# Kernel optimization log

Hardware: AMD Instinct MI355X
Metric: run time of the kernel (lower is better)

## Reference

```python
import jax, jax.numpy as jnp
import numpy as np
from jax import lax

MAX_DISP = 192
DOWNSAMPLE = 4
DEPTH = MAX_DISP // DOWNSAMPLE  # 48 disparity levels
B, C, H, W = 4, 512, 96, 320


def setup_inputs() -> dict:
    key = jax.random.key(0)
    k1, k2 = jax.random.split(key)
    left_features = jax.random.normal(k1, (B, C, H, W), dtype=jnp.float32)
    right_features = jax.random.normal(k2, (B, C, H, W), dtype=jnp.float32)
    return {"left_features": left_features, "right_features": right_features}


def _cost_volume(left, right):
    # cost[b, i, h, w] = mean_c left[b,c,h,w] * right[b,c,h,w-i]  for w >= i, else 0
    w_idx = jnp.arange(left.shape[3])

    def body(carry, i):
        r = jnp.roll(right, i, axis=3)            # right[..., w-i] (wrapped)
        corr = jnp.mean(left * r, axis=1)         # [B, H, W]
        corr = jnp.where(w_idx >= i, corr, jnp.float32(0.0))
        return carry, corr

    _, cost = lax.scan(body, None, jnp.arange(DEPTH))  # [D, B, H, W]
    return jnp.transpose(cost, (1, 0, 2, 3))           # [B, D, H, W]


def reference(left_features, right_features):
    return _cost_volume(left_features, right_features)
```

## Files before the change

kernel.cpp:

```cpp
#include <hip/hip_runtime.h>
#include <hip/hip_bf16.h>

#define B_ 4
#define C_ 512
#define H_ 96
#define W_ 320
#define D_ 48
#define HW_ (H_*W_)

#define KC 32
#define NCHUNK (C_/KC)
#define WCOLS 112
#define CSTR 72
#define LDSB (WCOLS*CSTR)
#define NT 64
#define NUW 224
#define SIT 4
#define EPS2 36

typedef __attribute__((ext_vector_type(8))) short bf16x8;
typedef __attribute__((ext_vector_type(4))) float f32x4;

__device__ __forceinline__ unsigned cvt2(float lo, float hi) {
  union { __hip_bfloat162 h2; unsigned u; } u;
  u.h2 = __float22bfloat162_rn(make_float2(lo, hi));
  return u.u;
}
__device__ __forceinline__ int ldsoff(int col, int q) {
  return col * CSTR + (q << 3);
}

__global__ __launch_bounds__(NT)
void cost_volume_mfma(const float* __restrict__ Lp,
                      const float* __restrict__ Rp,
                      float* __restrict__ out) {
  __shared__ __align__(16) char lds[LDSB];
  const int ln = threadIdx.x;
  const int bid = blockIdx.x;
  const int t2 = bid % 10;
  const int bh = bid / 10;
  const int b = bh / H_, h = bh % H_;
  const int lc = ln & 15;
  const int lg = (ln >> 4) & 3;
  const int m0 = 2 * t2;

  const float* sp[SIT];
  int dstb[SIT];
  bool sact[SIT];
#pragma unroll
  for (int it = 0; it < SIT; ++it) {
    const int u = ln + 64 * it;
    bool a = (u < NUW);
    const int uc = a ? u : 0;
    const int c4 = uc % 28, chq = uc / 28;
    const int col = 4 * c4;
    int x;
    const float* bp;
    if (c4 < 8) { x = 16 * m0 + col; bp = Lp; }
    else {
      const int dnp = (c4 - 8) >> 2, jn = m0 + 1 - dnp;
      x = 16 * jn + 4 * ((c4 - 8) & 3);
      bp = Rp;
      a = a && (jn >= 0);
    }
    if (x < 0) x = 0;
    sp[it] = bp + ((size_t)(b * C_ + 4 * chq) * H_ + h) * W_ + x;
    dstb[it] = ldsoff(col, chq);
    sact[it] = a;
  }

  float4 sreg[SIT][4];

#define SLOAD() \
  _Pragma("unroll") for (int it = 0; it < SIT; ++it) { \
    if (sact[it]) { \
      _Pragma("unroll") for (int l = 0; l < 4; ++l) \
        sreg[it][l] = *(const float4*)(sp[it] + (size_t)l * HW_); \
    } \
    sp[it] += (size_t)KC * HW_; \
  }

#define SWRITE() \
  _Pragma("unroll") for (int it = 0; it < SIT; ++it) if (sact[it]) { \
    char* p = lds + dstb[it]; \
    uint2 v; \
    v.x = cvt2(sreg[it][0].x, sreg[it][1].x); v.y = cvt2(sreg[it][2].x, sreg[it][3].x); \
    *(uint2*)(p) = v; \
    v.x = cvt2(sreg[it][0].y, sreg[it][1].y); v.y = cvt2(sreg[it][2].y, sreg[it][3].y); \
    *(uint2*)(p + CSTR) = v; \
    v.x = cvt2(sreg[it][0].z, sreg[it][1].z); v.y = cvt2(sreg[it][2].z, sreg[it][3].z); \
    *(uint2*)(p + 2 * CSTR) = v; \
    v.x = cvt2(sreg[it][0].w, sreg[it][1].w); v.y = cvt2(sreg[it][2].w, sreg[it][3].w); \
    *(uint2*)(p + 3 * CSTR) = v; \
  }

  const int aoff0 = ldsoff(lc, 2 * lg);
  const int aoff1 = ldsoff(16 + lc, 2 * lg);
  int boff[5];
  bool bval[5];
#pragma unroll
  for (int dnp = 0; dnp < 5; ++dnp) {
    boff[dnp] = ldsoff(32 + 16 * dnp + lc, 2 * lg);
    bval[dnp] = (m0 + 1 - dnp) >= 0;
  }

  union FragU { uint2 h[2]; bf16x8 v; };
#define FREAD(fr, off) do { FragU _f; \
  _f.h[0] = *(const uint2*)(lds + (off)); \
  _f.h[1] = *(const uint2*)(lds + (off) + 8); fr = _f.v; } while (0)

  f32x4 acc[2][4];
#pragma unroll
  for (int ml = 0; ml < 2; ++ml)
#pragma unroll
    for (int dn = 0; dn < 4; ++dn) acc[ml][dn] = (f32x4){0.f, 0.f, 0.f, 0.f};

  SLOAD();
  SWRITE();
  SLOAD();
  for (int k = 0; k < NCHUNK; ++k) {
    bf16x8 a0, a1;
    FREAD(a0, aoff0);
    FREAD(a1, aoff1);
    bf16x8 bf[5];
#pragma unroll
    for (int dnp = 0; dnp < 5; ++dnp)
      if (bval[dnp]) FREAD(bf[dnp], boff[dnp]);
#pragma unroll
    for (int dn = 0; dn < 4; ++dn) {
      if (bval[dn + 1])
        acc[0][dn] = __builtin_amdgcn_mfma_f32_16x16x32_bf16(a0, bf[dn + 1], acc[0][dn], 0, 0, 0);
      if (bval[dn])
        acc[1][dn] = __builtin_amdgcn_mfma_f32_16x16x32_bf16(a1, bf[dn], acc[1][dn], 0, 0, 0);
    }
    if (k < NCHUNK - 1) SWRITE();
    if (k < NCHUNK - 2) SLOAD();
  }

  __syncthreads();
  float* ep = (float*)lds;
#pragma unroll
  for (int e = 0; e < (D_ * EPS2 + NT - 1) / NT; ++e) {
    const int i = ln + NT * e;
    if (i < D_ * EPS2) ep[i] = 0.f;
  }
  __syncthreads();
  const float scale = 1.f / 512.f;
#pragma unroll
  for (int ml = 0; ml < 2; ++ml) {
#pragma unroll
    for (int dn = 0; dn < 4; ++dn) {
      if ((m0 + ml - dn) >= 0) {
#pragma unroll
        for (int q = 0; q < 4; ++q) {
          const int i = 4 * lg + q;
          const int d = 16 * dn + i - lc;
          if (d >= 0 && d < D_)
            ep[d * EPS2 + 16 * ml + i] = acc[ml][dn][q] * scale;
        }
      }
    }
  }
  __syncthreads();
#pragma unroll
  for (int e = 0; e < 6; ++e) {
    const int u = ln + NT * e;
    const int d = u >> 3, c4 = u & 7;
    const float4 v = *(const float4*)(ep + d * EPS2 + 4 * c4);
    float* o = out + (((size_t)b * D_ + d) * H_ + h) * W_ + 16 * m0 + 4 * c4;
    *(float4*)o = v;
  }
}

extern "C" void kernel_launch(void* const* d_in, const int* in_sizes, int n_in,
                              void* d_out, int out_size, void* d_ws, size_t ws_size,
                              hipStream_t stream) {
  const float* left  = (const float*)d_in[0];
  const float* right = (const float*)d_in[1];
  float* outp = (float*)d_out;
  cost_volume_mfma<<<dim3(B_ * H_ * 10), dim3(NT), 0, stream>>>(left, right, outp);
}
```

Before: 142.3 us.

## Double-buffer global prefetch registers and remap block IDs across XCDs

```diff
diff --git a/kernel.cpp b/kernel.cpp
--- a/kernel.cpp
+++ b/kernel.cpp
@@ -17,6 +17,7 @@
 #define NUW 224
 #define SIT 4
 #define EPS2 36
+#define NBLK (B_*H_*10)
 
 typedef __attribute__((ext_vector_type(8))) short bf16x8;
 typedef __attribute__((ext_vector_type(4))) float f32x4;
@@ -37,14 +38,16 @@
   __shared__ __align__(16) char lds[LDSB];
   const int ln = threadIdx.x;
   const int bid = blockIdx.x;
-  const int t2 = bid % 10;
-  const int bh = bid / 10;
+  const int wk = (bid & 7) * (NBLK / 8) + (bid >> 3);
+  const int t2 = wk % 10;
+  const int bh = wk / 10;
   const int b = bh / H_, h = bh % H_;
   const int lc = ln & 15;
   const int lg = (ln >> 4) & 3;
   const int m0 = 2 * t2;
 
-  const float* sp[SIT];
+  const float* spA[SIT];
+  const float* spB[SIT];
   int dstb[SIT];
   bool sact[SIT];
 #pragma unroll
@@ -64,33 +67,34 @@
       a = a && (jn >= 0);
     }
     if (x < 0) x = 0;
-    sp[it] = bp + ((size_t)(b * C_ + 4 * chq) * H_ + h) * W_ + x;
+    spA[it] = bp + ((size_t)(b * C_ + 4 * chq) * H_ + h) * W_ + x;
+    spB[it] = spA[it] + (size_t)KC * HW_;
     dstb[it] = ldsoff(col, chq);
     sact[it] = a;
   }
 
-  float4 sreg[SIT][4];
+  float4 srA[SIT][4], srB[SIT][4];
 
-#define SLOAD() \
+#define SLOADX(sr, sp) \
   _Pragma("unroll") for (int it = 0; it < SIT; ++it) { \
     if (sact[it]) { \
       _Pragma("unroll") for (int l = 0; l < 4; ++l) \
-        sreg[it][l] = *(const float4*)(sp[it] + (size_t)l * HW_); \
+        sr[it][l] = *(const float4*)(sp[it] + (size_t)l * HW_); \
     } \
-    sp[it] += (size_t)KC * HW_; \
+    sp[it] += (size_t)2 * KC * HW_; \
   }
 
-#define SWRITE() \
+#define SWRITEX(sr) \
   _Pragma("unroll") for (int it = 0; it < SIT; ++it) if (sact[it]) { \
     char* p = lds + dstb[it]; \
     uint2 v; \
-    v.x = cvt2(sreg[it][0].x, sreg[it][1].x); v.y = cvt2(sreg[it][2].x, sreg[it][3].x); \
+    v.x = cvt2(sr[it][0].x, sr[it][1].x); v.y = cvt2(sr[it][2].x, sr[it][3].x); \
     *(uint2*)(p) = v; \
-    v.x = cvt2(sreg[it][0].y, sreg[it][1].y); v.y = cvt2(sreg[it][2].y, sreg[it][3].y); \
+    v.x = cvt2(sr[it][0].y, sr[it][1].y); v.y = cvt2(sr[it][2].y, sr[it][3].y); \
     *(uint2*)(p + CSTR) = v; \
-    v.x = cvt2(sreg[it][0].z, sreg[it][1].z); v.y = cvt2(sreg[it][2].z, sreg[it][3].z); \
+    v.x = cvt2(sr[it][0].z, sr[it][1].z); v.y = cvt2(sr[it][2].z, sr[it][3].z); \
     *(uint2*)(p + 2 * CSTR) = v; \
-    v.x = cvt2(sreg[it][0].w, sreg[it][1].w); v.y = cvt2(sreg[it][2].w, sreg[it][3].w); \
+    v.x = cvt2(sr[it][0].w, sr[it][1].w); v.y = cvt2(sr[it][2].w, sr[it][3].w); \
     *(uint2*)(p + 3 * CSTR) = v; \
   }
 
@@ -115,26 +119,32 @@
 #pragma unroll
     for (int dn = 0; dn < 4; ++dn) acc[ml][dn] = (f32x4){0.f, 0.f, 0.f, 0.f};
 
-  SLOAD();
-  SWRITE();
-  SLOAD();
-  for (int k = 0; k < NCHUNK; ++k) {
-    bf16x8 a0, a1;
-    FREAD(a0, aoff0);
-    FREAD(a1, aoff1);
-    bf16x8 bf[5];
-#pragma unroll
-    for (int dnp = 0; dnp < 5; ++dnp)
-      if (bval[dnp]) FREAD(bf[dnp], boff[dnp]);
-#pragma unroll
-    for (int dn = 0; dn < 4; ++dn) {
-      if (bval[dn + 1])
-        acc[0][dn] = __builtin_amdgcn_mfma_f32_16x16x32_bf16(a0, bf[dn + 1], acc[0][dn], 0, 0, 0);
-      if (bval[dn])
-        acc[1][dn] = __builtin_amdgcn_mfma_f32_16x16x32_bf16(a1, bf[dn], acc[1][dn], 0, 0, 0);
-    }
-    if (k < NCHUNK - 1) SWRITE();
-    if (k < NCHUNK - 2) SLOAD();
+#define COMPUTE() do { \
+    bf16x8 a0, a1; \
+    FREAD(a0, aoff0); \
+    FREAD(a1, aoff1); \
+    bf16x8 bf[5]; \
+    _Pragma("unroll") for (int dnp = 0; dnp < 5; ++dnp) \
+      if (bval[dnp]) FREAD(bf[dnp], boff[dnp]); \
+    _Pragma("unroll") for (int dn = 0; dn < 4; ++dn) { \
+      if (bval[dn + 1]) \
+        acc[0][dn] = __builtin_amdgcn_mfma_f32_16x16x32_bf16(a0, bf[dn + 1], acc[0][dn], 0, 0, 0); \
+      if (bval[dn]) \
+        acc[1][dn] = __builtin_amdgcn_mfma_f32_16x16x32_bf16(a1, bf[dn], acc[1][dn], 0, 0, 0); \
+    } \
+  } while (0)
+
+  SLOADX(srA, spA);
+  SWRITEX(srA);
+  SLOADX(srB, spB);
+  SLOADX(srA, spA);
+  for (int k = 0; k < NCHUNK; k += 2) {
+    COMPUTE();
+    SWRITEX(srB);
+    if (k + 3 < NCHUNK) SLOADX(srB, spB);
+    COMPUTE();
+    if (k + 2 < NCHUNK) SWRITEX(srA);
+    if (k + 4 < NCHUNK) SLOADX(srA, spA);
   }
 
   __syncthreads();
@@ -178,5 +188,5 @@
   const float* left  = (const float*)d_in[0];
   const float* right = (const float*)d_in[1];
   float* outp = (float*)d_out;
-  cost_volume_mfma<<<dim3(B_ * H_ * 10), dim3(NT), 0, stream>>>(left, right, outp);
+  cost_volume_mfma<<<dim3(NBLK), dim3(NT), 0, stream>>>(left, right, outp);
 }
```

Result: slower. 191.2 us (+34.3%).
